# Performance work log

Measured on AMD Instinct MI355X. Metric: run time of the kernel, lower is better.

Reference implementation:

```python
import jax, jax.numpy as jnp
import numpy as np

N = 100000

def _gcn_norm(edge_index, n):
    # PyG GCNConv default: add self-loops, symmetric deg^-1/2 normalization
    loops = jnp.arange(n, dtype=edge_index.dtype)
    src = jnp.concatenate([edge_index[0], loops])
    dst = jnp.concatenate([edge_index[1], loops])
    deg = jax.ops.segment_sum(jnp.ones_like(dst, dtype=jnp.float32), dst, num_segments=n)
    dinv = jnp.where(deg > 0, jax.lax.rsqrt(deg), 0.0)
    norm = dinv[src] * dinv[dst]  # [E+N]
    return src, dst, norm

def _gcn_conv(h, W, b, src, dst, norm, n):
    # transform then gather-scale-scatter aggregate
    h = h @ W                                   # [N, out]
    out = jax.ops.segment_sum(norm[:, None] * h[src], dst, num_segments=n)
    return out + b

def _prelu(h, a):
    return jnp.where(h > 0, h, a * h)

def _dropout(h, u, p=0.5):
    # deterministic dropout: keep where u >= p, scale by 1/(1-p)
    return jnp.where(u >= p, h / (1.0 - p), 0.0)

def setup_inputs() -> dict:
    key = jax.random.key(0)
    ks = jax.random.split(key, 12)
    D, H1, H2, C, E = 512, 128, 16, 10, 1600000
    x = jax.random.normal(ks[0], (N, D), dtype=jnp.float32)
    edge_index = jax.random.randint(ks[1], (2, E), 0, N, dtype=jnp.int64)
    u1 = jax.random.uniform(ks[2], (N, H1), dtype=jnp.float32)
    u2 = jax.random.uniform(ks[3], (N, H2), dtype=jnp.float32)
    def glorot(k, shp):
        lim = np.sqrt(6.0 / (shp[0] + shp[1]))
        return jax.random.uniform(k, shp, dtype=jnp.float32, minval=-lim, maxval=lim)
    W1 = glorot(ks[4], (D, H1)); b1 = jnp.zeros((H1,), jnp.float32)
    W2 = glorot(ks[5], (H1, H2)); b2 = jnp.zeros((H2,), jnp.float32)
    fcW = glorot(ks[6], (H2, C)); fcb = jnp.zeros((C,), jnp.float32)
    a = jnp.float32(0.25)  # PReLU init (shared single param for both layers)
    return {"x": x, "edge_index": edge_index, "W1": W1, "b1": b1, "W2": W2,
            "b2": b2, "a": a, "fcW": fcW, "fcb": fcb, "u1": u1, "u2": u2}

def reference(x, edge_index, W1, b1, W2, b2, a, fcW, fcb, u1, u2):
    src, dst, norm = _gcn_norm(edge_index, N)
    feat1 = _dropout(_prelu(_gcn_conv(x, W1, b1, src, dst, norm, N), a), u1)
    feat2 = _dropout(_prelu(_gcn_conv(feat1, W2, b2, src, dst, norm, N), a), u2)
    logits = feat2 @ fcW + fcb
    return (feat2, logits)
```

## Files before the change

kernel.cpp:

```cpp
#include <hip/hip_runtime.h>
#include <hip/hip_bf16.h>
#include <stdint.h>

#define NN 100000
#define DIN 512
#define H1C 128
#define H2C 16
#define NCLS 10
#define NB_SCAN ((NN + 255) / 256)

typedef __attribute__((ext_vector_type(8))) short s16x8;
typedef __attribute__((ext_vector_type(4))) float f32x4;
typedef __attribute__((ext_vector_type(4))) unsigned short u16x4;
typedef __attribute__((ext_vector_type(8))) unsigned short u16x8;

static __device__ __forceinline__ unsigned short f2bf(float f) {
  __hip_bfloat16 h = __float2bfloat16(f);
  return *(unsigned short*)&h;
}
static __device__ __forceinline__ float bflo(unsigned u) {
  return __uint_as_float(u << 16);
}
static __device__ __forceinline__ float bfhi(unsigned u) {
  return __uint_as_float(u & 0xffff0000u);
}

__device__ __forceinline__ int ld_src(const int* __restrict__ ei, int f, int E, int i) {
  return f ? ei[2 * (size_t)i] : ei[i];
}
__device__ __forceinline__ int ld_dst(const int* __restrict__ ei, int f, int E, int i) {
  return f ? ei[2 * ((size_t)E + (size_t)i)] : ei[(size_t)E + (size_t)i];
}

__global__ void k_pre(const int* __restrict__ ei, int* __restrict__ flag,
                      int* __restrict__ deg,
                      const float* __restrict__ W1, unsigned short* __restrict__ Wt, int n) {
  int i = blockIdx.x * 256 + threadIdx.x;
  if (blockIdx.x == 0 && threadIdx.x < 64) {
    int v = ei[2 * threadIdx.x + 1];
    unsigned long long b = __ballot(v == 0);
    if (threadIdx.x == 0) *flag = (b == ~0ull) ? 1 : 0;
  }
  if (i < n) deg[i] = 0;
  if (i < H1C * DIN) {
    int nn = i >> 9, k = i & 511;
    Wt[i] = f2bf(W1[(size_t)k * H1C + nn]);
  }
}

__global__ void k_count(const int* __restrict__ ei, const int* __restrict__ flag,
                        int E, int* __restrict__ deg, int* __restrict__ rank) {
  int i = blockIdx.x * blockDim.x + threadIdx.x;
  if (i >= E) return;
  int f = *flag;
  rank[i] = atomicAdd(&deg[ld_dst(ei, f, E, i)], 1);
}

__global__ void k_scanA(const int* __restrict__ deg, int* __restrict__ incl,
                        int* __restrict__ bsum, float* __restrict__ dinv, int n) {
  __shared__ int s[256];
  int i = blockIdx.x * 256 + threadIdx.x;
  int v = (i < n) ? deg[i] : 0;
  if (i < n) dinv[i] = rsqrtf((float)(v + 1));
  s[threadIdx.x] = v;
  __syncthreads();
  for (int off = 1; off < 256; off <<= 1) {
    int t = (threadIdx.x >= off) ? s[threadIdx.x - off] : 0;
    __syncthreads();
    s[threadIdx.x] += t;
    __syncthreads();
  }
  if (i < n) incl[i] = s[threadIdx.x];
  if (threadIdx.x == 255) bsum[blockIdx.x] = s[255];
}

__global__ void k_scanB(int* __restrict__ bsum, int nb) {
  __shared__ int s[512];
  int v = (threadIdx.x < nb) ? bsum[threadIdx.x] : 0;
  s[threadIdx.x] = v;
  __syncthreads();
  for (int off = 1; off < 512; off <<= 1) {
    int t = (threadIdx.x >= off) ? s[threadIdx.x - off] : 0;
    __syncthreads();
    s[threadIdx.x] += t;
    __syncthreads();
  }
  if (threadIdx.x < nb) bsum[threadIdx.x] = s[threadIdx.x] - v;
}

__global__ void k_scanC(const int* __restrict__ deg, const int* __restrict__ bsum,
                        int* __restrict__ offs, int n, int E) {
  int i = blockIdx.x * 256 + threadIdx.x;
  if (i < n) offs[i] = offs[i] - deg[i] + bsum[i >> 8];
  if (i == 0) offs[n] = E;
}

__global__ void k_scatter(const int* __restrict__ ei, const int* __restrict__ flag, int E,
                          const int* __restrict__ offs, const int* __restrict__ rank,
                          const float* __restrict__ dinv, uint2* __restrict__ csr_sw) {
  int i = blockIdx.x * blockDim.x + threadIdx.x;
  if (i >= E) return;
  int f = *flag;
  int s = ld_src(ei, f, E, i), d = ld_dst(ei, f, E, i);
  int pos = offs[d] + rank[i];
  uint2 rec;
  rec.x = (unsigned)s;
  rec.y = __float_as_uint(dinv[s]);
  csr_sw[pos] = rec;
}

#define BM 64
#define BK 64
#define LDA 72
#define LDB 72

__global__ __launch_bounds__(256) void k_gemm1_mfma(const float* __restrict__ x,
                                                    const unsigned short* __restrict__ Wt,
                                                    unsigned int* __restrict__ h1u, int n) {
  __shared__ unsigned short As[BM * LDA];
  __shared__ unsigned short Bs[H1C * LDB];
  int tid = threadIdx.x;
  int wave = tid >> 6, lane = tid & 63;
  int wm = wave >> 1, wn = wave & 1;
  int bm = blockIdx.x * BM;
  int lrow = lane & 15, lk = (lane >> 4) * 8;

  f32x4 acc[2][4];
#pragma unroll
  for (int i = 0; i < 2; i++)
#pragma unroll
    for (int j = 0; j < 4; j++) acc[i][j] = (f32x4){0.f, 0.f, 0.f, 0.f};

  float4 areg[4];
  u16x8 breg[4];

  auto loadA = [&](int k0) {
#pragma unroll
    for (int p = 0; p < 4; p++) {
      int idx = p * 256 + tid;
      int r = idx >> 4, c4 = (idx & 15) * 4;
      int row = bm + r;
      areg[p] = make_float4(0.f, 0.f, 0.f, 0.f);
      if (row < n) areg[p] = *(const float4*)(x + (size_t)row * DIN + k0 + c4);
    }
  };
  auto loadB = [&](int k0) {
#pragma unroll
    for (int p = 0; p < 4; p++) {
      int idx = p * 256 + tid;
      int r = idx >> 3, c8 = (idx & 7) * 8;
      breg[p] = *(const u16x8*)&Wt[(size_t)r * DIN + k0 + c8];
    }
  };

  loadA(0);
  loadB(0);

  for (int k0 = 0; k0 < DIN; k0 += BK) {
#pragma unroll
    for (int p = 0; p < 4; p++) {
      int idx = p * 256 + tid;
      int r = idx >> 4, c4 = (idx & 15) * 4;
      u16x4 b4;
      b4.x = f2bf(areg[p].x); b4.y = f2bf(areg[p].y);
      b4.z = f2bf(areg[p].z); b4.w = f2bf(areg[p].w);
      *(u16x4*)&As[r * LDA + c4] = b4;
      int rb = idx >> 3, c8 = (idx & 7) * 8;
      int pr = (rb & 64) + (((rb & 1) + 2 * ((rb >> 5) & 1)) << 4) + ((rb >> 1) & 15);
      *(u16x8*)&Bs[pr * LDB + c8] = breg[p];
    }
    if (k0 + BK < DIN) {
      loadA(k0 + BK);
      loadB(k0 + BK);
    }
    __syncthreads();
#pragma unroll
    for (int kk = 0; kk < 2; kk++) {
      s16x8 a[2], b[4];
#pragma unroll
      for (int mi = 0; mi < 2; mi++)
        a[mi] = *(const s16x8*)&As[(wm * 32 + mi * 16 + lrow) * LDA + kk * 32 + lk];
#pragma unroll
      for (int nj = 0; nj < 4; nj++)
        b[nj] = *(const s16x8*)&Bs[(wn * 64 + nj * 16 + lrow) * LDB + kk * 32 + lk];
#pragma unroll
      for (int mi = 0; mi < 2; mi++)
#pragma unroll
        for (int nj = 0; nj < 4; nj++)
          acc[mi][nj] = __builtin_amdgcn_mfma_f32_16x16x32_bf16(a[mi], b[nj], acc[mi][nj], 0, 0, 0);
    }
    __syncthreads();
  }
#pragma unroll
  for (int mi = 0; mi < 2; mi++) {
#pragma unroll
    for (int r = 0; r < 4; r++) {
      int row = bm + wm * 32 + mi * 16 + (lane >> 4) * 4 + r;
      if (row < n) {
        unsigned p0 = ((unsigned)f2bf(acc[mi][1][r]) << 16) | (unsigned)f2bf(acc[mi][0][r]);
        unsigned p1 = ((unsigned)f2bf(acc[mi][3][r]) << 16) | (unsigned)f2bf(acc[mi][2][r]);
        h1u[(size_t)row * 64 + wn * 32 + lrow] = p0;
        h1u[(size_t)row * 64 + wn * 32 + 16 + lrow] = p1;
      }
    }
  }
}

__global__ __launch_bounds__(256) void k_agg1(const unsigned int* __restrict__ h1u,
                                              const uint2* __restrict__ csr_sw,
                                              const int* __restrict__ offs,
                                              const float* __restrict__ dinv,
                                              const float* __restrict__ b1,
                                              const float* __restrict__ aP,
                                              const float* __restrict__ u1,
                                              unsigned int* __restrict__ f1u, int n) {
  int wid = (blockIdx.x * 256 + threadIdx.x) >> 6;
  int lane = threadIdx.x & 63;
  if (wid >= n) return;
  int d = wid;
  int beg = offs[d], end = offs[d + 1];
  unsigned gs = h1u[(size_t)d * 64 + lane];
  float ax = 0.f, ay = 0.f;
  int e = beg;
  for (; e + 7 < end; e += 8) {
    uint2 r0 = csr_sw[e],     r1 = csr_sw[e + 1], r2 = csr_sw[e + 2], r3 = csr_sw[e + 3];
    uint2 r4 = csr_sw[e + 4], r5 = csr_sw[e + 5], r6 = csr_sw[e + 6], r7 = csr_sw[e + 7];
    unsigned g0 = h1u[(size_t)r0.x * 64 + lane];
    unsigned g1 = h1u[(size_t)r1.x * 64 + lane];
    unsigned g2 = h1u[(size_t)r2.x * 64 + lane];
    unsigned g3 = h1u[(size_t)r3.x * 64 + lane];
    unsigned g4 = h1u[(size_t)r4.x * 64 + lane];
    unsigned g5 = h1u[(size_t)r5.x * 64 + lane];
    unsigned g6 = h1u[(size_t)r6.x * 64 + lane];
    unsigned g7 = h1u[(size_t)r7.x * 64 + lane];
    float w0 = __uint_as_float(r0.y), w1 = __uint_as_float(r1.y);
    float w2 = __uint_as_float(r2.y), w3 = __uint_as_float(r3.y);
    float w4 = __uint_as_float(r4.y), w5 = __uint_as_float(r5.y);
    float w6 = __uint_as_float(r6.y), w7 = __uint_as_float(r7.y);
    ax += w0 * bflo(g0); ay += w0 * bfhi(g0);
    ax += w1 * bflo(g1); ay += w1 * bfhi(g1);
    ax += w2 * bflo(g2); ay += w2 * bfhi(g2);
    ax += w3 * bflo(g3); ay += w3 * bfhi(g3);
    ax += w4 * bflo(g4); ay += w4 * bfhi(g4);
    ax += w5 * bflo(g5); ay += w5 * bfhi(g5);
    ax += w6 * bflo(g6); ay += w6 * bfhi(g6);
    ax += w7 * bflo(g7); ay += w7 * bfhi(g7);
  }
  for (; e + 3 < end; e += 4) {
    uint2 r0 = csr_sw[e], r1 = csr_sw[e + 1], r2 = csr_sw[e + 2], r3 = csr_sw[e + 3];
    unsigned g0 = h1u[(size_t)r0.x * 64 + lane];
    unsigned g1 = h1u[(size_t)r1.x * 64 + lane];
    unsigned g2 = h1u[(size_t)r2.x * 64 + lane];
    unsigned g3 = h1u[(size_t)r3.x * 64 + lane];
    float w0 = __uint_as_float(r0.y), w1 = __uint_as_float(r1.y);
    float w2 = __uint_as_float(r2.y), w3 = __uint_as_float(r3.y);
    ax += w0 * bflo(g0); ay += w0 * bfhi(g0);
    ax += w1 * bflo(g1); ay += w1 * bfhi(g1);
    ax += w2 * bflo(g2); ay += w2 * bfhi(g2);
    ax += w3 * bflo(g3); ay += w3 * bfhi(g3);
  }
  for (; e < end; e++) {
    uint2 rr = csr_sw[e];
    float w = __uint_as_float(rr.y);
    unsigned g = h1u[(size_t)rr.x * 64 + lane];
    ax += w * bflo(g); ay += w * bfhi(g);
  }
  float di = dinv[d];
  ax = (ax + di * bflo(gs)) * di;
  ay = (ay + di * bfhi(gs)) * di;
  float2 bb = ((const float2*)b1)[lane];
  ax += bb.x; ay += bb.y;
  float al = *aP;
  ax = ax > 0.f ? ax : al * ax;
  ay = ay > 0.f ? ay : al * ay;
  float2 uu = ((const float2*)u1)[(size_t)d * 64 + lane];
  ax = (uu.x >= 0.5f) ? ax * 2.f : 0.f;
  ay = (uu.y >= 0.5f) ? ay * 2.f : 0.f;
  unsigned pk = ((unsigned)f2bf(ay) << 16) | (unsigned)f2bf(ax);
  f1u[(size_t)d * 64 + lane] = pk;
}

__global__ __launch_bounds__(256) void k_gemm2(const unsigned int* __restrict__ f1u,
                                               const float* __restrict__ W2,
                                               unsigned int* __restrict__ h2u, int n) {
  __shared__ float ws[H1C][H2C];
  __shared__ unsigned int fs[16][66];
  int tid = threadIdx.x;
#pragma unroll
  for (int p = 0; p < 8; p++) {
    int idx = tid + p * 256;
    ws[idx >> 4][idx & 15] = W2[idx];
  }
  int r0 = blockIdx.x * 16;
  {
    int r = tid >> 4, c4 = (tid & 15) * 4;
    int row = r0 + r;
    uint4 v = make_uint4(0, 0, 0, 0);
    if (row < n) v = *(const uint4*)(f1u + (size_t)row * 64 + c4);
    *(uint4*)&fs[r][c4] = v;
  }
  __syncthreads();
  int col = tid & 15, r = tid >> 4;
  float acc = 0.f;
#pragma unroll
  for (int k = 0; k < 64; k++) {
    unsigned u = fs[r][k];
    acc += bflo(u) * ws[2 * k][col] + bfhi(u) * ws[2 * k + 1][col];
  }
  int row = r0 + r;
  float accN = __shfl_xor(acc, 1, 64);
  if ((col & 1) == 0 && row < n) {
    unsigned pk = ((unsigned)f2bf(accN) << 16) | (unsigned)f2bf(acc);
    h2u[(size_t)row * 8 + (col >> 1)] = pk;
  }
}

__global__ __launch_bounds__(256) void k_agg2(const unsigned int* __restrict__ h2u,
                                              const uint2* __restrict__ csr_sw,
                                              const int* __restrict__ offs,
                                              const float* __restrict__ dinv,
                                              const float* __restrict__ b2,
                                              const float* __restrict__ aP,
                                              const float* __restrict__ u2,
                                              const float* __restrict__ fcW,
                                              const float* __restrict__ fcb,
                                              float* __restrict__ out_feat2,
                                              float* __restrict__ out_logits, int n) {
  int wid = (blockIdx.x * 256 + threadIdx.x) >> 6;
  int lane = threadIdx.x & 63;
  if (wid >= n) return;
  int d = wid;
  int g = lane >> 3, j = lane & 7;
  int beg = offs[d], end = offs[d + 1];
  unsigned gs = h2u[(size_t)d * 8 + j];
  float aa = 0.f, ab = 0.f;
  int e = beg + g;
  for (; e + 8 < end; e += 16) {
    uint2 r0 = csr_sw[e], r1 = csr_sw[e + 8];
    unsigned g0 = h2u[(size_t)r0.x * 8 + j];
    unsigned g1 = h2u[(size_t)r1.x * 8 + j];
    float w0 = __uint_as_float(r0.y), w1 = __uint_as_float(r1.y);
    aa += w0 * bflo(g0) + w1 * bflo(g1);
    ab += w0 * bfhi(g0) + w1 * bfhi(g1);
  }
  for (; e < end; e += 8) {
    uint2 rr = csr_sw[e];
    unsigned gg = h2u[(size_t)rr.x * 8 + j];
    float w = __uint_as_float(rr.y);
    aa += w * bflo(gg); ab += w * bfhi(gg);
  }
  aa += __shfl_xor(aa, 8, 64); aa += __shfl_xor(aa, 16, 64); aa += __shfl_xor(aa, 32, 64);
  ab += __shfl_xor(ab, 8, 64); ab += __shfl_xor(ab, 16, 64); ab += __shfl_xor(ab, 32, 64);
  float di = dinv[d];
  aa = (aa + di * bflo(gs)) * di;
  ab = (ab + di * bfhi(gs)) * di;
  aa += b2[2 * j]; ab += b2[2 * j + 1];
  float al = *aP;
  aa = aa > 0.f ? aa : al * aa;
  ab = ab > 0.f ? ab : al * ab;
  float2 uu = ((const float2*)(u2 + (size_t)d * H2C))[j];
  aa = (uu.x >= 0.5f) ? aa * 2.f : 0.f;
  ab = (uu.y >= 0.5f) ? ab * 2.f : 0.f;
  if (lane < 8) {
    float2 o; o.x = aa; o.y = ab;
    ((float2*)(out_feat2 + (size_t)d * H2C))[j] = o;
  }
  int c = lane & 15;
  int cc = (c < NCLS) ? c : 0;
  float lg = fcb[cc];
#pragma unroll
  for (int k = 0; k < 8; k++) {
    float va = __shfl(aa, k, 64);
    float vb = __shfl(ab, k, 64);
    lg += va * fcW[(2 * k) * NCLS + cc] + vb * fcW[(2 * k + 1) * NCLS + cc];
  }
  if (lane < NCLS) out_logits[(size_t)d * NCLS + c] = lg;
}

extern "C" void kernel_launch(void* const* d_in, const int* in_sizes, int n_in,
                              void* d_out, int out_size, void* d_ws, size_t ws_size,
                              hipStream_t stream) {
  const float* x   = (const float*)d_in[0];
  const int*   ei  = (const int*)d_in[1];
  const float* W1  = (const float*)d_in[2];
  const float* b1  = (const float*)d_in[3];
  const float* W2  = (const float*)d_in[4];
  const float* b2  = (const float*)d_in[5];
  const float* aP  = (const float*)d_in[6];
  const float* fcW = (const float*)d_in[7];
  const float* fcb = (const float*)d_in[8];
  const float* u1  = (const float*)d_in[9];
  const float* u2  = (const float*)d_in[10];
  const int E = in_sizes[1] / 2;

  float* out_feat2  = (float*)d_out;
  float* out_logits = (float*)d_out + (size_t)NN * H2C;

  char* w = (char*)d_ws;
  size_t off = 0;
  auto A = [&](size_t bytes) -> char* {
    char* p = w + off;
    off = (off + bytes + 255) & ~(size_t)255;
    return p;
  };
  int*   flag   = (int*)A(256);
  int*   deg    = (int*)A((size_t)NN * 4);
  int*   offs   = (int*)A((size_t)(NN + 1) * 4);
  float* dinv   = (float*)A((size_t)NN * 4);
  int*   bsum   = (int*)A(512 * 4);
  int*   rank   = (int*)A((size_t)E * 4);
  uint2* csr_sw = (uint2*)A((size_t)E * 8);
  unsigned int* h1u = (unsigned int*)A((size_t)NN * 64 * 4);
  unsigned int* f1u = (unsigned int*)A((size_t)NN * 64 * 4);
  unsigned int* h2u = (unsigned int*)A((size_t)NN * 8 * 4);
  unsigned short* Wt = (unsigned short*)A((size_t)H1C * DIN * 2);

  dim3 b256(256);
  int gE = (E + 255) / 256;
  int gN = (NN + 255) / 256;

  k_pre<<<gN, b256, 0, stream>>>(ei, flag, deg, W1, Wt, NN);
  k_count<<<gE, b256, 0, stream>>>(ei, flag, E, deg, rank);
  k_scanA<<<NB_SCAN, b256, 0, stream>>>(deg, offs, bsum, dinv, NN);
  k_scanB<<<1, 512, 0, stream>>>(bsum, NB_SCAN);
  k_scanC<<<gN, b256, 0, stream>>>(deg, bsum, offs, NN, E);
  k_scatter<<<gE, b256, 0, stream>>>(ei, flag, E, offs, rank, dinv, csr_sw);
  k_gemm1_mfma<<<(NN + BM - 1) / BM, b256, 0, stream>>>(x, Wt, h1u, NN);
  k_agg1<<<(NN + 3) / 4, b256, 0, stream>>>(h1u, csr_sw, offs, dinv, b1, aP, u1, f1u, NN);
  k_gemm2<<<(NN + 15) / 16, b256, 0, stream>>>(f1u, W2, h2u, NN);
  k_agg2<<<(NN + 3) / 4, b256, 0, stream>>>(h2u, csr_sw, offs, dinv, b2, aP, u2,
                                            fcW, fcb, out_feat2, out_logits, NN);
}
```

Baseline: 325.0 us.

## Merge scan phases and co-launch CSR scatter with first GEMM

Folds the second and third scan phases into one kernel: every block redundantly scans the block sums in shared memory and then applies its own offset. The CSR scatter is merged into the first MFMA GEMM launch as extra blocks, so the independent scatter and GEMM work can run at the same time on the GPU. This removes two kernel launches and lets scatter overlap the GEMM. In exchange, each of the ~391 scan blocks repeats the 512-entry scan, and the combined kernel's register and LDS footprint now also applies to the scatter blocks.

```diff
diff --git a/kernel.cpp b/kernel.cpp
--- a/kernel.cpp
+++ b/kernel.cpp
@@ -74,52 +74,59 @@
   if (threadIdx.x == 255) bsum[blockIdx.x] = s[255];
 }
 
-__global__ void k_scanB(int* __restrict__ bsum, int nb) {
+__global__ void k_scanBC(const int* __restrict__ deg, const int* __restrict__ bsum,
+                         int* __restrict__ offs, int n, int E, int nb) {
   __shared__ int s[512];
-  int v = (threadIdx.x < nb) ? bsum[threadIdx.x] : 0;
-  s[threadIdx.x] = v;
+  int tid = threadIdx.x;
+  int v = (tid < nb) ? bsum[tid] : 0;
+  s[tid] = v;
   __syncthreads();
   for (int off = 1; off < 512; off <<= 1) {
-    int t = (threadIdx.x >= off) ? s[threadIdx.x - off] : 0;
-    __syncthreads();
-    s[threadIdx.x] += t;
-    __syncthreads();
-  }
-  if (threadIdx.x < nb) bsum[threadIdx.x] = s[threadIdx.x] - v;
-}
-
-__global__ void k_scanC(const int* __restrict__ deg, const int* __restrict__ bsum,
-                        int* __restrict__ offs, int n, int E) {
-  int i = blockIdx.x * 256 + threadIdx.x;
-  if (i < n) offs[i] = offs[i] - deg[i] + bsum[i >> 8];
-  if (i == 0) offs[n] = E;
-}
-
-__global__ void k_scatter(const int* __restrict__ ei, const int* __restrict__ flag, int E,
-                          const int* __restrict__ offs, const int* __restrict__ rank,
-                          const float* __restrict__ dinv, uint2* __restrict__ csr_sw) {
-  int i = blockIdx.x * blockDim.x + threadIdx.x;
-  if (i >= E) return;
-  int f = *flag;
-  int s = ld_src(ei, f, E, i), d = ld_dst(ei, f, E, i);
-  int pos = offs[d] + rank[i];
-  uint2 rec;
-  rec.x = (unsigned)s;
-  rec.y = __float_as_uint(dinv[s]);
-  csr_sw[pos] = rec;
+    int t = (tid >= off) ? s[tid - off] : 0;
+    __syncthreads();
+    s[tid] += t;
+    __syncthreads();
+  }
+  int bid = blockIdx.x;
+  int pb = (bid > 0) ? s[bid - 1] : 0;
+  int i = bid * 256 + (tid & 255);
+  if (tid < 256 && i < n) offs[i] = offs[i] - deg[i] + pb;
+  if (bid == 0 && tid == 0) offs[n] = E;
 }
 
 #define BM 64
 #define BK 64
 #define LDA 72
 #define LDB 72
-
-__global__ __launch_bounds__(256) void k_gemm1_mfma(const float* __restrict__ x,
-                                                    const unsigned short* __restrict__ Wt,
-                                                    unsigned int* __restrict__ h1u, int n) {
+#define NGB ((NN + BM - 1) / BM)
+
+__global__ __launch_bounds__(256) void k_sg1(const float* __restrict__ x,
+                                             const unsigned short* __restrict__ Wt,
+                                             unsigned int* __restrict__ h1u, int n,
+                                             const int* __restrict__ ei,
+                                             const int* __restrict__ flag, int E,
+                                             const int* __restrict__ offs,
+                                             const int* __restrict__ rank,
+                                             const float* __restrict__ dinv,
+                                             uint2* __restrict__ csr_sw) {
   __shared__ unsigned short As[BM * LDA];
   __shared__ unsigned short Bs[H1C * LDB];
   int tid = threadIdx.x;
+
+  if (blockIdx.x >= NGB) {
+    int i = (blockIdx.x - NGB) * 256 + tid;
+    if (i < E) {
+      int f = *flag;
+      int s = ld_src(ei, f, E, i), d = ld_dst(ei, f, E, i);
+      int pos = offs[d] + rank[i];
+      uint2 rec;
+      rec.x = (unsigned)s;
+      rec.y = __float_as_uint(dinv[s]);
+      csr_sw[pos] = rec;
+    }
+    return;
+  }
+
   int wave = tid >> 6, lane = tid & 63;
   int wm = wave >> 1, wn = wave & 1;
   int bm = blockIdx.x * BM;
@@ -422,10 +429,8 @@
   k_pre<<<gN, b256, 0, stream>>>(ei, flag, deg, W1, Wt, NN);
   k_count<<<gE, b256, 0, stream>>>(ei, flag, E, deg, rank);
   k_scanA<<<NB_SCAN, b256, 0, stream>>>(deg, offs, bsum, dinv, NN);
-  k_scanB<<<1, 512, 0, stream>>>(bsum, NB_SCAN);
-  k_scanC<<<gN, b256, 0, stream>>>(deg, bsum, offs, NN, E);
-  k_scatter<<<gE, b256, 0, stream>>>(ei, flag, E, offs, rank, dinv, csr_sw);
-  k_gemm1_mfma<<<(NN + BM - 1) / BM, b256, 0, stream>>>(x, Wt, h1u, NN);
+  k_scanBC<<<NB_SCAN, 512, 0, stream>>>(deg, bsum, offs, NN, E, NB_SCAN);
+  k_sg1<<<NGB + gE, b256, 0, stream>>>(x, Wt, h1u, NN, ei, flag, E, offs, rank, dinv, csr_sw);
   k_agg1<<<(NN + 3) / 4, b256, 0, stream>>>(h1u, csr_sw, offs, dinv, b1, aP, u1, f1u, NN);
   k_gemm2<<<(NN + 15) / 16, b256, 0, stream>>>(f1u, W2, h2u, NN);
   k_agg2<<<(NN + 3) / 4, b256, 0, stream>>>(h2u, csr_sw, offs, dinv, b2, aP, u2,
```

New measurement: 322.2 us. About the same (-0.9%).
